# Kernel optimization log

Measured on AMD Instinct MI355X. Metric: run time of the kernel, lower is better.

## Reference

```python
import jax, jax.numpy as jnp
from jax import lax
import numpy as np

D_MODEL = 512
D_STATE = 16
D_CONV = 4
EXPAND = 2
D_INNER = EXPAND * D_MODEL
DT_RANK = (D_MODEL + 15) // 16  # ceil(d_model/16) = 32
B, L = 4, 1024


def setup_inputs() -> dict:
    key = jax.random.key(0)
    ks = jax.random.split(key, 12)
    s = 0.02
    inp = {
        "feature": jax.random.normal(ks[0], (B, L, D_MODEL), jnp.float32),
        "ln_w": jnp.ones((D_MODEL,), jnp.float32),
        "ln_b": jnp.zeros((D_MODEL,), jnp.float32),
        "in_proj_w": jax.random.normal(ks[1], (2 * D_INNER, D_MODEL), jnp.float32) * s,
        "conv_w": jax.random.normal(ks[2], (D_INNER, D_CONV), jnp.float32) * 0.1,
        "conv_b": jnp.zeros((D_INNER,), jnp.float32),
        "x_proj_w": jax.random.normal(ks[3], (DT_RANK + 2 * D_STATE, D_INNER), jnp.float32) * s,
        "dt_proj_w": jax.random.normal(ks[4], (D_INNER, DT_RANK), jnp.float32) * 0.1,
        "dt_proj_b": jax.random.normal(ks[5], (D_INNER,), jnp.float32) * 0.1 - 4.0,
        "A_log": jnp.log(jnp.broadcast_to(jnp.arange(1, D_STATE + 1, dtype=jnp.float32), (D_INNER, D_STATE))),
        "D": jnp.ones((D_INNER,), jnp.float32),
        "out_proj_w": jax.random.normal(ks[6], (D_MODEL, D_INNER), jnp.float32) * s,
    }
    return inp


def _mamba_block(xn, in_proj_w, conv_w, conv_b, x_proj_w, dt_proj_w, dt_proj_b, A_log, D, out_proj_w):
    # xn: [B, L, d_model]
    xz = jnp.einsum('bld,ed->ble', xn, in_proj_w)          # [B, L, 2*d_inner]
    x, z = xz[..., :D_INNER], xz[..., D_INNER:]
    # causal depthwise conv along L
    xc = jnp.transpose(x, (0, 2, 1))                        # [B, d_inner, L]
    xc = lax.conv_general_dilated(
        xc, conv_w[:, None, :], (1,), [(D_CONV - 1, 0)],
        feature_group_count=D_INNER,
        dimension_numbers=('NCH', 'OIH', 'NCH')) + conv_b[None, :, None]
    x = jax.nn.silu(jnp.transpose(xc, (0, 2, 1)))           # [B, L, d_inner]
    x_dbl = jnp.einsum('bld,ed->ble', x, x_proj_w)          # [B, L, dt_rank+2*d_state]
    dt = x_dbl[..., :DT_RANK]
    Bm = x_dbl[..., DT_RANK:DT_RANK + D_STATE]
    Cm = x_dbl[..., DT_RANK + D_STATE:]
    dt = jax.nn.softplus(jnp.einsum('blr,dr->bld', dt, dt_proj_w) + dt_proj_b)  # [B,L,d_inner]
    A = -jnp.exp(A_log)                                     # [d_inner, d_state]

    def step(h, inp):
        dt_t, B_t, C_t, x_t = inp                           # [B,d_inner],[B,d_state],[B,d_state],[B,d_inner]
        dA = jnp.exp(dt_t[..., None] * A)                   # [B, d_inner, d_state]
        h = dA * h + (dt_t * x_t)[..., None] * B_t[:, None, :]
        y = jnp.einsum('bds,bs->bd', h, C_t)
        return h, y

    xs = (jnp.transpose(dt, (1, 0, 2)), jnp.transpose(Bm, (1, 0, 2)),
          jnp.transpose(Cm, (1, 0, 2)), jnp.transpose(x, (1, 0, 2)))
    h0 = jnp.zeros((xn.shape[0], D_INNER, D_STATE), xn.dtype)
    _, ys = lax.scan(step, h0, xs)                          # ys: [L, B, d_inner]
    y = jnp.transpose(ys, (1, 0, 2)) + x * D
    y = y * jax.nn.silu(z)
    return jnp.einsum('bld,ed->ble', y, out_proj_w)         # [B, L, d_model]


def reference(feature, ln_w, ln_b, in_proj_w, conv_w, conv_b, x_proj_w,
              dt_proj_w, dt_proj_b, A_log, D, out_proj_w):
    eps = 1e-5
    mu = jnp.mean(feature, axis=-1, keepdims=True)
    var = jnp.var(feature, axis=-1, keepdims=True)
    xn = (feature - mu) / jnp.sqrt(var + eps) * ln_w + ln_b
    out = _mamba_block(xn, in_proj_w, conv_w, conv_b, x_proj_w,
                       dt_proj_w, dt_proj_b, A_log, D, out_proj_w)
    return xn + out
```

## Files before the change

kernel.cpp:

```cpp
#include <hip/hip_runtime.h>
#include <hip/hip_bf16.h>
#include <math.h>

#define B_SZ 4
#define L_SZ 1024
#define DM   512
#define DI   1024
#define DS   16
#define DTR  32
#define NXD  64
#define M_ROWS (B_SZ*L_SZ)
#define CHK  32
#define CLEN 32
#define NCH  (B_SZ*DI)
#define LDA  40

typedef __attribute__((ext_vector_type(8))) short short8;
typedef __attribute__((ext_vector_type(4))) float f32x4;
typedef __hip_bfloat16 bf16;

__device__ __forceinline__ float bf2f(bf16 x){ return __bfloat162float(x); }
__device__ __forceinline__ float fsig(float x){ return __builtin_amdgcn_rcpf(1.f + __expf(-x)); }
#define LOG2E 1.44269504f

__global__ void detect_kernel(const void* lnw, int* flag) {
    unsigned u = *(const unsigned*)lnw;
    *flag = (u == 0x3F800000u) ? 1 : 0;
}

__global__ void cvt_b16_all(const void* __restrict__ s0, const void* __restrict__ s1,
                            const void* __restrict__ s2, bf16* __restrict__ d0,
                            bf16* __restrict__ d1, bf16* __restrict__ d2,
                            const int* __restrict__ flag) {
    int n; const void* s; bf16* d;
    switch (blockIdx.y) {
        case 0:  n = 1048576; s = s0; d = d0; break;
        case 1:  n = 65536;   s = s1; d = d1; break;
        default: n = 524288;  s = s2; d = d2; break;
    }
    int i = blockIdx.x*256 + threadIdx.x;
    if (i >= n) return;
    if (*flag) d[i] = __float2bfloat16(((const float*)s)[i]);
    else       d[i] = ((const bf16*)s)[i];
}
__global__ void cvt_f32_all(const void* __restrict__ s0, const void* __restrict__ s1,
                            const void* __restrict__ s2, const void* __restrict__ s3,
                            const void* __restrict__ s4, const void* __restrict__ s5,
                            const void* __restrict__ s6, const void* __restrict__ s7,
                            float* __restrict__ d0, float* __restrict__ d1,
                            float* __restrict__ d2, float* __restrict__ d3,
                            float* __restrict__ d4, float* __restrict__ d5,
                            float* __restrict__ d6, float* __restrict__ d7,
                            const int* __restrict__ flag) {
    int n; const void* s; float* d;
    switch (blockIdx.y) {
        case 0:  n = 512;   s = s0; d = d0; break;
        case 1:  n = 512;   s = s1; d = d1; break;
        case 2:  n = 4096;  s = s2; d = d2; break;
        case 3:  n = 1024;  s = s3; d = d3; break;
        case 4:  n = 32768; s = s4; d = d4; break;
        case 5:  n = 1024;  s = s5; d = d5; break;
        case 6:  n = 16384; s = s6; d = d6; break;
        default: n = 1024;  s = s7; d = d7; break;
    }
    int i = blockIdx.x*256 + threadIdx.x;
    if (i >= n) return;
    float v;
    if (*flag) v = ((const float*)s)[i];
    else       v = bf2f(((const bf16*)s)[i]);
    if (blockIdx.y == 4) {
        d[(i & (DTR-1))*DI + (i >> 5)] = v;
    } else {
        d[i] = v;
    }
}

__global__ void ln_kernel(const void* __restrict__ f,
                          const float* __restrict__ w,
                          const float* __restrict__ b,
                          float* __restrict__ xn, bf16* __restrict__ xnb,
                          const int* __restrict__ flag) {
    int row = blockIdx.x;
    int t = threadIdx.x;
    int fl = *flag;
    size_t base = (size_t)row*DM;
    float v0, v1;
    if (fl) { v0 = ((const float*)f)[base+t]; v1 = ((const float*)f)[base+t+256]; }
    else    { v0 = bf2f(((const bf16*)f)[base+t]); v1 = bf2f(((const bf16*)f)[base+t+256]); }
    __shared__ float ssum[256], ssq[256];
    ssum[t] = v0+v1; ssq[t] = v0*v0+v1*v1;
    __syncthreads();
    for (int off=128; off>0; off>>=1){
        if (t<off){ ssum[t]+=ssum[t+off]; ssq[t]+=ssq[t+off]; }
        __syncthreads();
    }
    float mu  = ssum[0]*(1.0f/DM);
    float var = ssq[0]*(1.0f/DM) - mu*mu;
    float rstd = rsqrtf(var + 1e-5f);
    float o0 = (v0-mu)*rstd*w[t]     + b[t];
    float o1 = (v1-mu)*rstd*w[t+256] + b[t+256];
    xn[base + t]      = o0;
    xn[base + t+256]  = o1;
    xnb[base + t]     = __float2bfloat16(o0);
    xnb[base + t+256] = __float2bfloat16(o1);
}


__global__ __launch_bounds__(256) void gemm_in_mfma(const bf16* __restrict__ A,
        const bf16* __restrict__ W, bf16* __restrict__ XB, bf16* __restrict__ ZB) {
    const int K = 512;
    __shared__ bf16 As[128*LDA];
    __shared__ bf16 Bs[128*LDA];
    int t = threadIdx.x;
    int w = t>>6, l = t&63;
    int wm = w&1, wn = w>>1;
    int row0 = blockIdx.y*128, col0 = blockIdx.x*128;
    int lr = l&15, lq = l>>4;
    int srow = t>>2, scol = (t&3)*8;
    f32x4 acc[4][4] = {};
    for (int k0=0; k0<K; k0+=32) {
        short8 a0 = *(const short8*)(A + (size_t)(row0+srow)*K    + k0 + scol);
        short8 a1 = *(const short8*)(A + (size_t)(row0+64+srow)*K + k0 + scol);
        short8 b0 = *(const short8*)(W + (size_t)(col0+srow)*K    + k0 + scol);
        short8 b1 = *(const short8*)(W + (size_t)(col0+64+srow)*K + k0 + scol);
        __syncthreads();
        *(short8*)(As + srow*LDA + scol)      = a0;
        *(short8*)(As + (64+srow)*LDA + scol) = a1;
        *(short8*)(Bs + srow*LDA + scol)      = b0;
        *(short8*)(Bs + (64+srow)*LDA + scol) = b1;
        __syncthreads();
        short8 af[4], bfr[4];
        #pragma unroll
        for (int mi=0;mi<4;mi++) af[mi]  = *(const short8*)(As + (wm*64+mi*16+lr)*LDA + lq*8);
        #pragma unroll
        for (int ni=0;ni<4;ni++) bfr[ni] = *(const short8*)(Bs + (wn*64+ni*16+lr)*LDA + lq*8);
        #pragma unroll
        for (int mi=0;mi<4;mi++)
            #pragma unroll
            for (int ni=0;ni<4;ni++)
                acc[mi][ni] = __builtin_amdgcn_mfma_f32_16x16x32_bf16(af[mi], bfr[ni], acc[mi][ni], 0,0,0);
    }
    bf16* dst; int cb;
    if (col0 < DI) { dst = XB; cb = col0; } else { dst = ZB; cb = col0 - DI; }
    #pragma unroll
    for (int mi=0;mi<4;mi++)
        #pragma unroll
        for (int ni=0;ni<4;ni++) {
            int r = row0 + wm*64 + mi*16 + lq*4;
            int c = cb   + wn*64 + ni*16 + lr;
            #pragma unroll
            for (int rr=0;rr<4;rr++)
                dst[(size_t)(r+rr)*DI + c] = __float2bfloat16(acc[mi][ni][rr]);
        }
}

__global__ __launch_bounds__(256) void gemm_x_mfma(const bf16* __restrict__ A,
        const bf16* __restrict__ W, float* __restrict__ C) {
    const int K = 1024;
    __shared__ bf16 As[64*LDA];
    __shared__ bf16 Bs[64*LDA];
    int t = threadIdx.x;
    int w = t>>6, l = t&63;
    int wm = w&1, wn = w>>1;
    int row0 = blockIdx.y*64;
    int lr = l&15, lq = l>>4;
    int srow = t>>2, scol = (t&3)*8;
    f32x4 acc[2][2] = {};
    for (int k0=0; k0<K; k0+=32) {
        short8 a0 = *(const short8*)(A + (size_t)(row0+srow)*K + k0 + scol);
        short8 b0 = *(const short8*)(W + (size_t)srow*K        + k0 + scol);
        __syncthreads();
        *(short8*)(As + srow*LDA + scol) = a0;
        *(short8*)(Bs + srow*LDA + scol) = b0;
        __syncthreads();
        short8 af[2], bfr[2];
        #pragma unroll
        for (int mi=0;mi<2;mi++) af[mi]  = *(const short8*)(As + (wm*32+mi*16+lr)*LDA + lq*8);
        #pragma unroll
        for (int ni=0;ni<2;ni++) bfr[ni] = *(const short8*)(Bs + (wn*32+ni*16+lr)*LDA + lq*8);
        #pragma unroll
        for (int mi=0;mi<2;mi++)
            #pragma unroll
            for (int ni=0;ni<2;ni++)
                acc[mi][ni] = __builtin_amdgcn_mfma_f32_16x16x32_bf16(af[mi], bfr[ni], acc[mi][ni], 0,0,0);
    }
    #pragma unroll
    for (int mi=0;mi<2;mi++)
        #pragma unroll
        for (int ni=0;ni<2;ni++) {
            int r = row0 + wm*32 + mi*16 + lq*4;
            int c = wn*32 + ni*16 + lr;
            #pragma unroll
            for (int rr=0;rr<4;rr++)
                C[(size_t)(r+rr)*NXD + c] = acc[mi][ni][rr];
        }
}

__global__ __launch_bounds__(256) void gemm_out_mfma(const bf16* __restrict__ A,
        const bf16* __restrict__ W, const float* __restrict__ xn,
        void* __restrict__ out, const int* __restrict__ flag) {
    const int K = 1024;
    __shared__ bf16 As[128*LDA];
    __shared__ bf16 Bs[128*LDA];
    int t = threadIdx.x;
    int w = t>>6, l = t&63;
    int wm = w&1, wn = w>>1;
    int row0 = blockIdx.y*128, col0 = blockIdx.x*128;
    int lr = l&15, lq = l>>4;
    int srow = t>>2, scol = (t&3)*8;
    f32x4 acc[4][4] = {};
    for (int k0=0; k0<K; k0+=32) {
        short8 a0 = *(const short8*)(A + (size_t)(row0+srow)*K    + k0 + scol);
        short8 a1 = *(const short8*)(A + (size_t)(row0+64+srow)*K + k0 + scol);
        short8 b0 = *(const short8*)(W + (size_t)(col0+srow)*K    + k0 + scol);
        short8 b1 = *(const short8*)(W + (size_t)(col0+64+srow)*K + k0 + scol);
        __syncthreads();
        *(short8*)(As + srow*LDA + scol)      = a0;
        *(short8*)(As + (64+srow)*LDA + scol) = a1;
        *(short8*)(Bs + srow*LDA + scol)      = b0;
        *(short8*)(Bs + (64+srow)*LDA + scol) = b1;
        __syncthreads();
        short8 af[4], bfr[4];
        #pragma unroll
        for (int mi=0;mi<4;mi++) af[mi]  = *(const short8*)(As + (wm*64+mi*16+lr)*LDA + lq*8);
        #pragma unroll
        for (int ni=0;ni<4;ni++) bfr[ni] = *(const short8*)(Bs + (wn*64+ni*16+lr)*LDA + lq*8);
        #pragma unroll
        for (int mi=0;mi<4;mi++)
            #pragma unroll
            for (int ni=0;ni<4;ni++)
                acc[mi][ni] = __builtin_amdgcn_mfma_f32_16x16x32_bf16(af[mi], bfr[ni], acc[mi][ni], 0,0,0);
    }
    int f = *flag;
    #pragma unroll
    for (int mi=0;mi<4;mi++)
        #pragma unroll
        for (int ni=0;ni<4;ni++) {
            int r = row0 + wm*64 + mi*16 + lq*4;
            int c = col0 + wn*64 + ni*16 + lr;
            #pragma unroll
            for (int rr=0;rr<4;rr++) {
                float v = acc[mi][ni][rr] + xn[(size_t)(r+rr)*DM + c];
                if (f) ((float*)out)[(size_t)(r+rr)*DM + c] = v;
                else   ((bf16*)out)[(size_t)(r+rr)*DM + c] = __float2bfloat16(v);
            }
        }
}

__global__ void conv_silu(const bf16* __restrict__ xb, const float* __restrict__ cw,
                          const float* __restrict__ cb, bf16* __restrict__ xc) {
    int idx = blockIdx.x*256 + threadIdx.x;
    int d  = idx & (DI-1);
    int ml = idx >> 10;
    int l  = ml & (L_SZ-1);
    float4 cwv = *(const float4*)(cw + d*4);
    float acc = cb[d];
    const bf16* p = xb + (size_t)(ml-3)*DI + d;
    if (l >= 3) {
        acc += bf2f(p[0])*cwv.x + bf2f(p[DI])*cwv.y + bf2f(p[2*DI])*cwv.z + bf2f(p[3*DI])*cwv.w;
    } else {
        if (l >= 1) acc += bf2f(p[2*DI])*cwv.z;
        if (l >= 2) acc += bf2f(p[DI])*cwv.y;
        acc += bf2f(p[3*DI])*cwv.w;
    }
    xc[idx] = __float2bfloat16(acc * fsig(acc));
}

__global__ __launch_bounds__(256) void dt_kernel(const float* __restrict__ xdbl,
        const float* __restrict__ dtwT, const float* __restrict__ dtb,
        float* __restrict__ dtf) {
    int m0 = blockIdx.x*4;
    int d0 = threadIdx.x*4;
    float4 bias = *(const float4*)(dtb + d0);
    float4 a0 = bias, a1 = bias, a2 = bias, a3 = bias;
    const float* xr = xdbl + (size_t)m0*NXD;
    #pragma unroll 4
    for (int r=0; r<DTR; r++) {
        float4 wv = *(const float4*)(dtwT + r*DI + d0);
        float x0 = xr[r], x1 = xr[NXD+r], x2 = xr[2*NXD+r], x3 = xr[3*NXD+r];
        a0.x = fmaf(wv.x,x0,a0.x); a0.y = fmaf(wv.y,x0,a0.y); a0.z = fmaf(wv.z,x0,a0.z); a0.w = fmaf(wv.w,x0,a0.w);
        a1.x = fmaf(wv.x,x1,a1.x); a1.y = fmaf(wv.y,x1,a1.y); a1.z = fmaf(wv.z,x1,a1.z); a1.w = fmaf(wv.w,x1,a1.w);
        a2.x = fmaf(wv.x,x2,a2.x); a2.y = fmaf(wv.y,x2,a2.y); a2.z = fmaf(wv.z,x2,a2.z); a2.w = fmaf(wv.w,x2,a2.w);
        a3.x = fmaf(wv.x,x3,a3.x); a3.y = fmaf(wv.y,x3,a3.y); a3.z = fmaf(wv.z,x3,a3.z); a3.w = fmaf(wv.w,x3,a3.w);
    }
    float4 accs[4] = {a0, a1, a2, a3};
    #pragma unroll
    for (int mm=0; mm<4; mm++) {
        float4 v = accs[mm];
        v.x = (v.x > 20.f) ? v.x : __logf(1.f + __expf(v.x));
        v.y = (v.y > 20.f) ? v.y : __logf(1.f + __expf(v.y));
        v.z = (v.z > 20.f) ? v.z : __logf(1.f + __expf(v.z));
        v.w = (v.w > 20.f) ? v.w : __logf(1.f + __expf(v.w));
        *(float4*)(dtf + (size_t)(m0+mm)*DI + d0) = v;
    }
}


__global__ __launch_bounds__(256) void scan_p1(const float* __restrict__ dtf,
        const bf16* __restrict__ xc, const float* __restrict__ xdbl,
        const float* __restrict__ A_log, float* __restrict__ SP, float* __restrict__ PP) {
    int ch = blockIdx.x*256 + threadIdx.x;
    int j  = blockIdx.y;
    int d  = ch & (DI-1);
    int bu = __builtin_amdgcn_readfirstlane(ch >> 10);
    float a2[DS];
    {
        const float4* pa = (const float4*)(A_log + d*DS);
        #pragma unroll
        for (int q=0;q<4;q++){
            float4 v = pa[q];
            a2[q*4+0] = -__expf(v.x)*LOG2E; a2[q*4+1] = -__expf(v.y)*LOG2E;
            a2[q*4+2] = -__expf(v.z)*LOG2E; a2[q*4+3] = -__expf(v.w)*LOG2E;
        }
    }
    float h[DS], P[DS];
    #pragma unroll
    for (int s=0;s<DS;s++){ h[s]=0.f; P[s]=1.f; }
    size_t row = (size_t)bu*L_SZ + (size_t)j*CLEN;
    const float* pdt = dtf + row*DI + d;
    const bf16*  pxc = xc  + row*DI + d;
    const float* pB  = xdbl + row*NXD + DTR;
    #pragma unroll 2
    for (int t=0; t<CLEN; t++) {
        float dt = *pdt;
        float u  = dt * bf2f(*pxc);
        #pragma unroll
        for (int s=0;s<DS;s++){
            float dA = __builtin_exp2f(dt*a2[s]);
            h[s] = fmaf(dA, h[s], u*pB[s]);
            P[s] *= dA;
        }
        pdt += DI; pxc += DI; pB += NXD;
    }
    float* sp = SP + ((size_t)j*NCH + ch)*DS;
    float* pp = PP + ((size_t)j*NCH + ch)*DS;
    #pragma unroll
    for (int q=0;q<4;q++){
        *(float4*)(sp + q*4) = make_float4(h[q*4], h[q*4+1], h[q*4+2], h[q*4+3]);
        *(float4*)(pp + q*4) = make_float4(P[q*4], P[q*4+1], P[q*4+2], P[q*4+3]);
    }
}

__global__ void scan_p2(const float* __restrict__ SP, const float* __restrict__ PP,
                        float* __restrict__ HB) {
    int idx = blockIdx.x*256 + threadIdx.x;
    float H = 0.f;
    for (int j=0;j<CHK;j++){
        size_t o = (size_t)j*(NCH*DS) + idx;
        float p = PP[o], s = SP[o];
        HB[o] = H;
        H = fmaf(p, H, s);
    }
}

__global__ __launch_bounds__(256) void scan_p3(const float* __restrict__ dtf,
        const bf16* __restrict__ xc, const float* __restrict__ xdbl,
        const float* __restrict__ A_log, const float* __restrict__ Dp,
        const float* __restrict__ HB, const bf16* __restrict__ zb,
        bf16* __restrict__ ybf) {
    int ch = blockIdx.x*256 + threadIdx.x;
    int j  = blockIdx.y;
    int d  = ch & (DI-1);
    int bu = __builtin_amdgcn_readfirstlane(ch >> 10);
    float a2[DS];
    {
        const float4* pa = (const float4*)(A_log + d*DS);
        #pragma unroll
        for (int q=0;q<4;q++){
            float4 v = pa[q];
            a2[q*4+0] = -__expf(v.x)*LOG2E; a2[q*4+1] = -__expf(v.y)*LOG2E;
            a2[q*4+2] = -__expf(v.z)*LOG2E; a2[q*4+3] = -__expf(v.w)*LOG2E;
        }
    }
    float h[DS];
    {
        const float4* ph = (const float4*)(HB + ((size_t)j*NCH + ch)*DS);
        #pragma unroll
        for (int q=0;q<4;q++){
            float4 v = ph[q];
            h[q*4]=v.x; h[q*4+1]=v.y; h[q*4+2]=v.z; h[q*4+3]=v.w;
        }
    }
    float Dd = Dp[d];
    size_t row = (size_t)bu*L_SZ + (size_t)j*CLEN;
    const float* pdt = dtf + row*DI + d;
    const bf16*  pxc = xc  + row*DI + d;
    const float* pB  = xdbl + row*NXD + DTR;
    const float* pC  = pB + DS;
    const bf16*  pz  = zb  + row*DI + d;
    bf16*        py  = ybf + row*DI + d;
    #pragma unroll 2
    for (int t=0; t<CLEN; t++) {
        float dt = *pdt;
        float xv = bf2f(*pxc);
        float u  = dt * xv;
        float y0=0.f, y1=0.f, y2=0.f, y3=0.f;
        #pragma unroll
        for (int s=0;s<DS;s+=4){
            float dA0 = __builtin_exp2f(dt*a2[s]);
            float dA1 = __builtin_exp2f(dt*a2[s+1]);
            float dA2 = __builtin_exp2f(dt*a2[s+2]);
            float dA3 = __builtin_exp2f(dt*a2[s+3]);
            h[s]   = fmaf(dA0, h[s],   u*pB[s]);
            h[s+1] = fmaf(dA1, h[s+1], u*pB[s+1]);
            h[s+2] = fmaf(dA2, h[s+2], u*pB[s+2]);
            h[s+3] = fmaf(dA3, h[s+3], u*pB[s+3]);
            y0 = fmaf(h[s],   pC[s],   y0);
            y1 = fmaf(h[s+1], pC[s+1], y1);
            y2 = fmaf(h[s+2], pC[s+2], y2);
            y3 = fmaf(h[s+3], pC[s+3], y3);
        }
        float y = (y0+y1) + (y2+y3) + xv*Dd;
        float z = bf2f(*pz);
        *py = __float2bfloat16(y * z * fsig(z));
        pdt += DI; pxc += DI; pB += NXD; pC += NXD; pz += DI; py += DI;
    }
}

extern "C" void kernel_launch(void* const* d_in, const int* in_sizes, int n_in,
                              void* d_out, int out_size, void* d_ws, size_t ws_size,
                              hipStream_t stream) {
    float* FW = (float*)d_ws;
    float* SP   = FW;
    float* PP   = FW + 2097152;
    float* HB   = FW + 4194304;
    bf16*  XNB  = (bf16*)(FW + 4194304);
    float* XN   = FW + 6291456;
    float* DTF  = FW + 8388608;
    float* XDBL = FW + 12582912;
    float* LNW  = FW + 12845056;
    float* LNB  = FW + 12845568;
    float* CW   = FW + 12846080;
    float* CB   = FW + 12850176;
    float* WDTT = FW + 12851200;
    float* BDT  = FW + 12883968;
    float* ALOG = FW + 12884992;
    float* DVEC = FW + 12901376;
    int*   FLAG = (int*)(FW + 12902400);
    bf16* XBB  = (bf16*)(FW + 12902912);
    bf16* YBF  = XBB;
    bf16* ZBB  = (bf16*)(FW + 15000064);
    bf16* XCB  = (bf16*)(FW + 17097216);
    bf16* WINB = (bf16*)(FW + 19194368);
    bf16* WXB  = (bf16*)(FW + 19718656);
    bf16* WOUTB= (bf16*)(FW + 19751424);

    detect_kernel<<<1, 1, 0, stream>>>(d_in[1], FLAG);

    cvt_b16_all<<<dim3(4096, 3), 256, 0, stream>>>(d_in[3], d_in[6], d_in[11],
                                                   WINB, WXB, WOUTB, FLAG);
    cvt_f32_all<<<dim3(128, 8), 256, 0, stream>>>(d_in[1], d_in[2], d_in[4], d_in[5],
                                                  d_in[7], d_in[8], d_in[9], d_in[10],
                                                  LNW, LNB, CW, CB, WDTT, BDT, ALOG, DVEC, FLAG);

    ln_kernel<<<M_ROWS, 256, 0, stream>>>(d_in[0], LNW, LNB, XN, XNB, FLAG);
    gemm_in_mfma<<<dim3(2048/128, M_ROWS/128), 256, 0, stream>>>(XNB, WINB, XBB, ZBB);
    conv_silu<<<M_ROWS*DI/256, 256, 0, stream>>>(XBB, CW, CB, XCB);
    gemm_x_mfma<<<dim3(1, M_ROWS/64), 256, 0, stream>>>(XCB, WXB, XDBL);
    dt_kernel<<<M_ROWS/4, 256, 0, stream>>>(XDBL, WDTT, BDT, DTF);
    scan_p1<<<dim3(NCH/256, CHK), 256, 0, stream>>>(DTF, XCB, XDBL, ALOG, SP, PP);
    scan_p2<<<(NCH*DS)/256, 256, 0, stream>>>(SP, PP, HB);
    scan_p3<<<dim3(NCH/256, CHK), 256, 0, stream>>>(DTF, XCB, XDBL, ALOG, DVEC, HB, ZBB, YBF);
    gemm_out_mfma<<<dim3(DM/128, M_ROWS/128), 256, 0, stream>>>(YBF, WOUTB, XN, d_out, FLAG);
}
```

Baseline: 253.9 us.

## Fuse prep kernels, prefetch GEMM tiles into registers, vectorize conv

```diff
diff --git a/kernel.cpp b/kernel.cpp
--- a/kernel.cpp
+++ b/kernel.cpp
@@ -23,86 +23,69 @@
 __device__ __forceinline__ float fsig(float x){ return __builtin_amdgcn_rcpf(1.f + __expf(-x)); }
 #define LOG2E 1.44269504f
 
-__global__ void detect_kernel(const void* lnw, int* flag) {
-    unsigned u = *(const unsigned*)lnw;
-    *flag = (u == 0x3F800000u) ? 1 : 0;
-}
-
-__global__ void cvt_b16_all(const void* __restrict__ s0, const void* __restrict__ s1,
-                            const void* __restrict__ s2, bf16* __restrict__ d0,
-                            bf16* __restrict__ d1, bf16* __restrict__ d2,
-                            const int* __restrict__ flag) {
-    int n; const void* s; bf16* d;
-    switch (blockIdx.y) {
-        case 0:  n = 1048576; s = s0; d = d0; break;
-        case 1:  n = 65536;   s = s1; d = d1; break;
-        default: n = 524288;  s = s2; d = d2; break;
-    }
-    int i = blockIdx.x*256 + threadIdx.x;
-    if (i >= n) return;
-    if (*flag) d[i] = __float2bfloat16(((const float*)s)[i]);
-    else       d[i] = ((const bf16*)s)[i];
-}
-__global__ void cvt_f32_all(const void* __restrict__ s0, const void* __restrict__ s1,
-                            const void* __restrict__ s2, const void* __restrict__ s3,
-                            const void* __restrict__ s4, const void* __restrict__ s5,
-                            const void* __restrict__ s6, const void* __restrict__ s7,
-                            float* __restrict__ d0, float* __restrict__ d1,
-                            float* __restrict__ d2, float* __restrict__ d3,
-                            float* __restrict__ d4, float* __restrict__ d5,
-                            float* __restrict__ d6, float* __restrict__ d7,
-                            const int* __restrict__ flag) {
-    int n; const void* s; float* d;
-    switch (blockIdx.y) {
-        case 0:  n = 512;   s = s0; d = d0; break;
-        case 1:  n = 512;   s = s1; d = d1; break;
-        case 2:  n = 4096;  s = s2; d = d2; break;
-        case 3:  n = 1024;  s = s3; d = d3; break;
-        case 4:  n = 32768; s = s4; d = d4; break;
-        case 5:  n = 1024;  s = s5; d = d5; break;
-        case 6:  n = 16384; s = s6; d = d6; break;
-        default: n = 1024;  s = s7; d = d7; break;
-    }
-    int i = blockIdx.x*256 + threadIdx.x;
-    if (i >= n) return;
-    float v;
-    if (*flag) v = ((const float*)s)[i];
-    else       v = bf2f(((const bf16*)s)[i]);
-    if (blockIdx.y == 4) {
-        d[(i & (DTR-1))*DI + (i >> 5)] = v;
+__device__ __forceinline__ bool is_f32(const void* lnw){
+    return *(const unsigned*)lnw == 0x3F800000u;
+}
+__device__ __forceinline__ float loadf(const void* s, int i, bool f){
+    return f ? ((const float*)s)[i] : bf2f(((const bf16*)s)[i]);
+}
+__device__ __forceinline__ bf16 loadb(const void* s, int i, bool f){
+    return f ? __float2bfloat16(((const float*)s)[i]) : ((const bf16*)s)[i];
+}
+__device__ __forceinline__ float4 loadw4(const void* s, int d, bool f){
+    if (f) return ((const float4*)s)[d];
+    uint2 u = ((const uint2*)s)[d];
+    float4 r;
+    r.x = __uint_as_float(u.x << 16); r.y = __uint_as_float(u.x & 0xffff0000u);
+    r.z = __uint_as_float(u.y << 16); r.w = __uint_as_float(u.y & 0xffff0000u);
+    return r;
+}
+
+#define CVT_TOTAL 1689600
+__global__ __launch_bounds__(256) void prep_kernel(
+        const void* __restrict__ feat, const void* __restrict__ lnw, const void* __restrict__ lnb,
+        const void* __restrict__ w_in, const void* __restrict__ w_x, const void* __restrict__ w_out,
+        const void* __restrict__ w_dt, const void* __restrict__ b_dt,
+        const void* __restrict__ alog, const void* __restrict__ dvec,
+        bf16* __restrict__ WINB, bf16* __restrict__ WXB, bf16* __restrict__ WOUTB,
+        float* __restrict__ WDTT, float* __restrict__ BDT, float* __restrict__ ALOG,
+        float* __restrict__ DVEC, float* __restrict__ xn, bf16* __restrict__ xnb) {
+    bool f = is_f32(lnw);
+    if (blockIdx.y == 0) {
+        int id = blockIdx.x*256 + threadIdx.x;
+        #pragma unroll 2
+        for (int g = id; g < CVT_TOTAL; g += 1048576) {
+            if      (g < 1048576)  WINB[g] = loadb(w_in, g, f);
+            else if (g < 1114112)  WXB[g-1048576] = loadb(w_x, g-1048576, f);
+            else if (g < 1638400)  WOUTB[g-1114112] = loadb(w_out, g-1114112, f);
+            else if (g < 1671168){ int i = g-1638400; WDTT[(i&(DTR-1))*DI + (i>>5)] = loadf(w_dt, i, f); }
+            else if (g < 1672192)  BDT[g-1671168] = loadf(b_dt, g-1671168, f);
+            else if (g < 1688576)  ALOG[g-1672192] = loadf(alog, g-1672192, f);
+            else                   DVEC[g-1688576] = loadf(dvec, g-1688576, f);
+        }
     } else {
-        d[i] = v;
-    }
-}
-
-__global__ void ln_kernel(const void* __restrict__ f,
-                          const float* __restrict__ w,
-                          const float* __restrict__ b,
-                          float* __restrict__ xn, bf16* __restrict__ xnb,
-                          const int* __restrict__ flag) {
-    int row = blockIdx.x;
-    int t = threadIdx.x;
-    int fl = *flag;
-    size_t base = (size_t)row*DM;
-    float v0, v1;
-    if (fl) { v0 = ((const float*)f)[base+t]; v1 = ((const float*)f)[base+t+256]; }
-    else    { v0 = bf2f(((const bf16*)f)[base+t]); v1 = bf2f(((const bf16*)f)[base+t+256]); }
-    __shared__ float ssum[256], ssq[256];
-    ssum[t] = v0+v1; ssq[t] = v0*v0+v1*v1;
-    __syncthreads();
-    for (int off=128; off>0; off>>=1){
-        if (t<off){ ssum[t]+=ssum[t+off]; ssq[t]+=ssq[t+off]; }
-        __syncthreads();
-    }
-    float mu  = ssum[0]*(1.0f/DM);
-    float var = ssq[0]*(1.0f/DM) - mu*mu;
-    float rstd = rsqrtf(var + 1e-5f);
-    float o0 = (v0-mu)*rstd*w[t]     + b[t];
-    float o1 = (v1-mu)*rstd*w[t+256] + b[t+256];
-    xn[base + t]      = o0;
-    xn[base + t+256]  = o1;
-    xnb[base + t]     = __float2bfloat16(o0);
-    xnb[base + t+256] = __float2bfloat16(o1);
+        int row = blockIdx.x;
+        int t = threadIdx.x;
+        size_t base = (size_t)row*DM;
+        float v0 = loadf(feat, base+t, f);
+        float v1 = loadf(feat, base+t+256, f);
+        __shared__ float ssum[256], ssq[256];
+        ssum[t] = v0+v1; ssq[t] = v0*v0+v1*v1;
+        __syncthreads();
+        for (int off=128; off>0; off>>=1){
+            if (t<off){ ssum[t]+=ssum[t+off]; ssq[t]+=ssq[t+off]; }
+            __syncthreads();
+        }
+        float mu  = ssum[0]*(1.0f/DM);
+        float var = ssq[0]*(1.0f/DM) - mu*mu;
+        float rstd = rsqrtf(var + 1e-5f);
+        float o0 = (v0-mu)*rstd*loadf(lnw,t,f)     + loadf(lnb,t,f);
+        float o1 = (v1-mu)*rstd*loadf(lnw,t+256,f) + loadf(lnb,t+256,f);
+        xn[base + t]      = o0;
+        xn[base + t+256]  = o1;
+        xnb[base + t]     = __float2bfloat16(o0);
+        xnb[base + t+256] = __float2bfloat16(o1);
+    }
 }
 
 
@@ -117,18 +100,28 @@
     int row0 = blockIdx.y*128, col0 = blockIdx.x*128;
     int lr = l&15, lq = l>>4;
     int srow = t>>2, scol = (t&3)*8;
+    const bf16* pA0 = A + (size_t)(row0+srow)*K    + scol;
+    const bf16* pA1 = A + (size_t)(row0+64+srow)*K + scol;
+    const bf16* pB0 = W + (size_t)(col0+srow)*K    + scol;
+    const bf16* pB1 = W + (size_t)(col0+64+srow)*K + scol;
     f32x4 acc[4][4] = {};
+    short8 a0 = *(const short8*)(pA0);
+    short8 a1 = *(const short8*)(pA1);
+    short8 b0 = *(const short8*)(pB0);
+    short8 b1 = *(const short8*)(pB1);
     for (int k0=0; k0<K; k0+=32) {
-        short8 a0 = *(const short8*)(A + (size_t)(row0+srow)*K    + k0 + scol);
-        short8 a1 = *(const short8*)(A + (size_t)(row0+64+srow)*K + k0 + scol);
-        short8 b0 = *(const short8*)(W + (size_t)(col0+srow)*K    + k0 + scol);
-        short8 b1 = *(const short8*)(W + (size_t)(col0+64+srow)*K + k0 + scol);
         __syncthreads();
         *(short8*)(As + srow*LDA + scol)      = a0;
         *(short8*)(As + (64+srow)*LDA + scol) = a1;
         *(short8*)(Bs + srow*LDA + scol)      = b0;
         *(short8*)(Bs + (64+srow)*LDA + scol) = b1;
         __syncthreads();
+        if (k0 + 32 < K) {
+            a0 = *(const short8*)(pA0 + k0 + 32);
+            a1 = *(const short8*)(pA1 + k0 + 32);
+            b0 = *(const short8*)(pB0 + k0 + 32);
+            b1 = *(const short8*)(pB1 + k0 + 32);
+        }
         short8 af[4], bfr[4];
         #pragma unroll
         for (int mi=0;mi<4;mi++) af[mi]  = *(const short8*)(As + (wm*64+mi*16+lr)*LDA + lq*8);
@@ -165,14 +158,20 @@
     int row0 = blockIdx.y*64;
     int lr = l&15, lq = l>>4;
     int srow = t>>2, scol = (t&3)*8;
+    const bf16* pA0 = A + (size_t)(row0+srow)*K + scol;
+    const bf16* pB0 = W + (size_t)srow*K        + scol;
     f32x4 acc[2][2] = {};
+    short8 a0 = *(const short8*)(pA0);
+    short8 b0 = *(const short8*)(pB0);
     for (int k0=0; k0<K; k0+=32) {
-        short8 a0 = *(const short8*)(A + (size_t)(row0+srow)*K + k0 + scol);
-        short8 b0 = *(const short8*)(W + (size_t)srow*K        + k0 + scol);
         __syncthreads();
         *(short8*)(As + srow*LDA + scol) = a0;
         *(short8*)(Bs + srow*LDA + scol) = b0;
         __syncthreads();
+        if (k0 + 32 < K) {
+            a0 = *(const short8*)(pA0 + k0 + 32);
+            b0 = *(const short8*)(pB0 + k0 + 32);
+        }
         short8 af[2], bfr[2];
         #pragma unroll
         for (int mi=0;mi<2;mi++) af[mi]  = *(const short8*)(As + (wm*32+mi*16+lr)*LDA + lq*8);
@@ -198,7 +197,7 @@
 
 __global__ __launch_bounds__(256) void gemm_out_mfma(const bf16* __restrict__ A,
         const bf16* __restrict__ W, const float* __restrict__ xn,
-        void* __restrict__ out, const int* __restrict__ flag) {
+        void* __restrict__ out, const void* __restrict__ lnw) {
     const int K = 1024;
     __shared__ bf16 As[128*LDA];
     __shared__ bf16 Bs[128*LDA];
@@ -208,18 +207,28 @@
     int row0 = blockIdx.y*128, col0 = blockIdx.x*128;
     int lr = l&15, lq = l>>4;
     int srow = t>>2, scol = (t&3)*8;
+    const bf16* pA0 = A + (size_t)(row0+srow)*K    + scol;
+    const bf16* pA1 = A + (size_t)(row0+64+srow)*K + scol;
+    const bf16* pB0 = W + (size_t)(col0+srow)*K    + scol;
+    const bf16* pB1 = W + (size_t)(col0+64+srow)*K + scol;
     f32x4 acc[4][4] = {};
+    short8 a0 = *(const short8*)(pA0);
+    short8 a1 = *(const short8*)(pA1);
+    short8 b0 = *(const short8*)(pB0);
+    short8 b1 = *(const short8*)(pB1);
     for (int k0=0; k0<K; k0+=32) {
-        short8 a0 = *(const short8*)(A + (size_t)(row0+srow)*K    + k0 + scol);
-        short8 a1 = *(const short8*)(A + (size_t)(row0+64+srow)*K + k0 + scol);
-        short8 b0 = *(const short8*)(W + (size_t)(col0+srow)*K    + k0 + scol);
-        short8 b1 = *(const short8*)(W + (size_t)(col0+64+srow)*K + k0 + scol);
         __syncthreads();
         *(short8*)(As + srow*LDA + scol)      = a0;
         *(short8*)(As + (64+srow)*LDA + scol) = a1;
         *(short8*)(Bs + srow*LDA + scol)      = b0;
         *(short8*)(Bs + (64+srow)*LDA + scol) = b1;
         __syncthreads();
+        if (k0 + 32 < K) {
+            a0 = *(const short8*)(pA0 + k0 + 32);
+            a1 = *(const short8*)(pA1 + k0 + 32);
+            b0 = *(const short8*)(pB0 + k0 + 32);
+            b1 = *(const short8*)(pB1 + k0 + 32);
+        }
         short8 af[4], bfr[4];
         #pragma unroll
         for (int mi=0;mi<4;mi++) af[mi]  = *(const short8*)(As + (wm*64+mi*16+lr)*LDA + lq*8);
@@ -231,7 +240,7 @@
             for (int ni=0;ni<4;ni++)
                 acc[mi][ni] = __builtin_amdgcn_mfma_f32_16x16x32_bf16(af[mi], bfr[ni], acc[mi][ni], 0,0,0);
     }
-    int f = *flag;
+    bool f = is_f32(lnw);
     #pragma unroll
     for (int mi=0;mi<4;mi++)
         #pragma unroll
@@ -247,23 +256,40 @@
         }
 }
 
-__global__ void conv_silu(const bf16* __restrict__ xb, const float* __restrict__ cw,
-                          const float* __restrict__ cb, bf16* __restrict__ xc) {
+__global__ __launch_bounds__(256) void conv_silu(const bf16* __restrict__ xb,
+        const void* __restrict__ cw, const void* __restrict__ cb,
+        bf16* __restrict__ xc, const void* __restrict__ lnw) {
+    bool f = is_f32(lnw);
     int idx = blockIdx.x*256 + threadIdx.x;
-    int d  = idx & (DI-1);
-    int ml = idx >> 10;
+    int dp = idx & (DI/2 - 1);
+    int d  = dp*2;
+    int ml = idx >> 9;
     int l  = ml & (L_SZ-1);
-    float4 cwv = *(const float4*)(cw + d*4);
-    float acc = cb[d];
-    const bf16* p = xb + (size_t)(ml-3)*DI + d;
+    float4 w0 = loadw4(cw, d,   f);
+    float4 w1 = loadw4(cw, d+1, f);
+    float acc0 = loadf(cb, d,   f);
+    float acc1 = loadf(cb, d+1, f);
+    const uint* p = (const uint*)(xb + (size_t)(ml-3)*DI + d);
+    const int S = DI/2;
+    float2 t0, t1, t2, t3;
+    #define UNPK(u) make_float2(__uint_as_float((u)<<16), __uint_as_float((u)&0xffff0000u))
     if (l >= 3) {
-        acc += bf2f(p[0])*cwv.x + bf2f(p[DI])*cwv.y + bf2f(p[2*DI])*cwv.z + bf2f(p[3*DI])*cwv.w;
+        t0 = UNPK(p[0]); t1 = UNPK(p[S]); t2 = UNPK(p[2*S]); t3 = UNPK(p[3*S]);
+        acc0 += t0.x*w0.x + t1.x*w0.y + t2.x*w0.z + t3.x*w0.w;
+        acc1 += t0.y*w1.x + t1.y*w1.y + t2.y*w1.z + t3.y*w1.w;
     } else {
-        if (l >= 1) acc += bf2f(p[2*DI])*cwv.z;
-        if (l >= 2) acc += bf2f(p[DI])*cwv.y;
-        acc += bf2f(p[3*DI])*cwv.w;
-    }
-    xc[idx] = __float2bfloat16(acc * fsig(acc));
+        t3 = UNPK(p[3*S]);
+        acc0 += t3.x*w0.w; acc1 += t3.y*w1.w;
+        if (l >= 1){ t2 = UNPK(p[2*S]); acc0 += t2.x*w0.z; acc1 += t2.y*w1.z; }
+        if (l >= 2){ t1 = UNPK(p[S]);   acc0 += t1.x*w0.y; acc1 += t1.y*w1.y; }
+    }
+    #undef UNPK
+    float y0 = acc0 * fsig(acc0);
+    float y1 = acc1 * fsig(acc1);
+    __hip_bfloat162 pk;
+    pk.x = __float2bfloat16(y0);
+    pk.y = __float2bfloat16(y1);
+    *(__hip_bfloat162*)(xc + (size_t)ml*DI + d) = pk;
 }
 
 __global__ __launch_bounds__(256) void dt_kernel(const float* __restrict__ xdbl,
@@ -428,15 +454,10 @@
     float* XN   = FW + 6291456;
     float* DTF  = FW + 8388608;
     float* XDBL = FW + 12582912;
-    float* LNW  = FW + 12845056;
-    float* LNB  = FW + 12845568;
-    float* CW   = FW + 12846080;
-    float* CB   = FW + 12850176;
     float* WDTT = FW + 12851200;
     float* BDT  = FW + 12883968;
     float* ALOG = FW + 12884992;
     float* DVEC = FW + 12901376;
-    int*   FLAG = (int*)(FW + 12902400);
     bf16* XBB  = (bf16*)(FW + 12902912);
     bf16* YBF  = XBB;
     bf16* ZBB  = (bf16*)(FW + 15000064);
@@ -445,21 +466,15 @@
     bf16* WXB  = (bf16*)(FW + 19718656);
     bf16* WOUTB= (bf16*)(FW + 19751424);
 
-    detect_kernel<<<1, 1, 0, stream>>>(d_in[1], FLAG);
-
-    cvt_b16_all<<<dim3(4096, 3), 256, 0, stream>>>(d_in[3], d_in[6], d_in[11],
-                                                   WINB, WXB, WOUTB, FLAG);
-    cvt_f32_all<<<dim3(128, 8), 256, 0, stream>>>(d_in[1], d_in[2], d_in[4], d_in[5],
-                                                  d_in[7], d_in[8], d_in[9], d_in[10],
-                                                  LNW, LNB, CW, CB, WDTT, BDT, ALOG, DVEC, FLAG);
-
-    ln_kernel<<<M_ROWS, 256, 0, stream>>>(d_in[0], LNW, LNB, XN, XNB, FLAG);
+    prep_kernel<<<dim3(4096, 2), 256, 0, stream>>>(
+        d_in[0], d_in[1], d_in[2], d_in[3], d_in[6], d_in[11], d_in[7], d_in[8],
+        d_in[9], d_in[10], WINB, WXB, WOUTB, WDTT, BDT, ALOG, DVEC, XN, XNB);
     gemm_in_mfma<<<dim3(2048/128, M_ROWS/128), 256, 0, stream>>>(XNB, WINB, XBB, ZBB);
-    conv_silu<<<M_ROWS*DI/256, 256, 0, stream>>>(XBB, CW, CB, XCB);
+    conv_silu<<<M_ROWS*DI/512, 256, 0, stream>>>(XBB, d_in[4], d_in[5], XCB, d_in[1]);
     gemm_x_mfma<<<dim3(1, M_ROWS/64), 256, 0, stream>>>(XCB, WXB, XDBL);
     dt_kernel<<<M_ROWS/4, 256, 0, stream>>>(XDBL, WDTT, BDT, DTF);
     scan_p1<<<dim3(NCH/256, CHK), 256, 0, stream>>>(DTF, XCB, XDBL, ALOG, SP, PP);
     scan_p2<<<(NCH*DS)/256, 256, 0, stream>>>(SP, PP, HB);
     scan_p3<<<dim3(NCH/256, CHK), 256, 0, stream>>>(DTF, XCB, XDBL, ALOG, DVEC, HB, ZBB, YBF);
-    gemm_out_mfma<<<dim3(DM/128, M_ROWS/128), 256, 0, stream>>>(YBF, WOUTB, XN, d_out, FLAG);
-}
+    gemm_out_mfma<<<dim3(DM/128, M_ROWS/128), 256, 0, stream>>>(YBF, WOUTB, XN, d_out, d_in[1]);
+}
```

Result: faster. 236.8 us (-6.7%).
